# Kernel tuning notes

Hardware: AMD Instinct MI355X
Metric: run time of the kernel (lower is better)

Reference implementation:

```python
import jax, jax.numpy as jnp
import numpy as np

K = 3  # knnLoss default k


def _knn_loss(source_pc, target_pc, k=K):
    """Faithful translation of knnLoss.forward.

    For each batch: drop exact-zero (0,0,0) points from both clouds
    (emulated via masking for static shapes), find the k nearest *target*
    points for every *source* point (query=source, ref=target), take the
    mean Euclidean distance, then average over batch.
    """

    def per_batch(src, tgt):  # src, tgt: [N, 3]
        src_valid = jnp.any(src != 0.0, axis=-1)  # [Ns] move_zero_point mask
        tgt_valid = jnp.any(tgt != 0.0, axis=-1)  # [Nt]
        s2 = jnp.sum(src * src, axis=-1)          # [Ns]
        t2 = jnp.sum(tgt * tgt, axis=-1)          # [Nt]
        # squared pairwise distances, [Ns, Nt]
        d2 = s2[:, None] + t2[None, :] - 2.0 * (src @ tgt.T)
        d2 = jnp.maximum(d2, 0.0)
        # invalid (zero) target points can never be a neighbor
        d2 = jnp.where(tgt_valid[None, :], d2, jnp.inf)
        neg_top, _ = jax.lax.top_k(-d2, k)        # k smallest squared dists
        dist = jnp.sqrt(-neg_top)                 # [Ns, k] euclidean, like KNN_CUDA
        # mean over valid source points x k neighbors
        num = jnp.sum(jnp.where(src_valid[:, None], dist, 0.0))
        den = jnp.sum(src_valid).astype(dist.dtype) * k
        return num / den

    return jnp.mean(jax.vmap(per_batch)(source_pc, target_pc))


def setup_inputs() -> dict:
    key = jax.random.key(0)
    k1, k2 = jax.random.split(key)
    B, N = 4, 8192
    source_pc = jax.random.normal(k1, (B, N, 3), dtype=jnp.float32)
    target_pc = jax.random.normal(k2, (B, N, 3), dtype=jnp.float32)
    return {"source_pc": source_pc, "target_pc": target_pc}


def reference(source_pc, target_pc):
    return _knn_loss(source_pc, target_pc)
```

## Files before the change

### kernel.cpp

```cpp
#include <hip/hip_runtime.h>
#include <math.h>

#define BATCH 4
#define NPTS 8192
#define TILE 512
#define TSPLIT 16
#define SRC_PER_BLOCK 512
#define SRC_CHUNKS 16
#define NSRC_TOT (BATCH * NPTS)
#define NOCT (TILE / 8)
#define OCTF 36

typedef __attribute__((ext_vector_type(2))) float f2;

__device__ __forceinline__ float min3f(float a, float b, float c) {
    float d;
    asm("v_min3_f32 %0, %1, %2, %3" : "=v"(d) : "v"(a), "v"(b), "v"(c));
    return d;
}

__device__ __forceinline__ void insert3(float d, float& a0, float& a1, float& a2) {
    float h = fmaxf(a1, d);
    float m = __builtin_amdgcn_fmed3f(a0, a1, d);
    a2 = fminf(a2, h);
    a1 = m;
    a0 = fminf(a0, d);
}

__device__ __forceinline__ void merge33(float a0, float a1, float a2,
                                        float& b0, float& b1, float& b2) {
    float s0 = fminf(a0, b0);
    float h  = fmaxf(a0, b0);
    float m  = fminf(a1, b1);
    float mm = fminf(a2, b2);
    b1 = fminf(h, m);
    b2 = __builtin_amdgcn_fmed3f(h, m, mm);
    b0 = s0;
}

__device__ __forceinline__ void octet_insert(const float4* ob, f2 nx, f2 ny, f2 nz,
                                             float& c0, float& c1, float& c2) {
    float4 X0 = ob[0], X1 = ob[1], Y0 = ob[2], Y1 = ob[3];
    float4 Z0 = ob[4], Z1 = ob[5], W0 = ob[6], W1 = ob[7];
    f2 pa = __builtin_elementwise_fma((f2){Z0.x, Z0.y}, nz, (f2){W0.x, W0.y});
    pa = __builtin_elementwise_fma((f2){Y0.x, Y0.y}, ny, pa);
    pa = __builtin_elementwise_fma((f2){X0.x, X0.y}, nx, pa);
    f2 pb = __builtin_elementwise_fma((f2){Z0.z, Z0.w}, nz, (f2){W0.z, W0.w});
    pb = __builtin_elementwise_fma((f2){Y0.z, Y0.w}, ny, pb);
    pb = __builtin_elementwise_fma((f2){X0.z, X0.w}, nx, pb);
    f2 pc = __builtin_elementwise_fma((f2){Z1.x, Z1.y}, nz, (f2){W1.x, W1.y});
    pc = __builtin_elementwise_fma((f2){Y1.x, Y1.y}, ny, pc);
    pc = __builtin_elementwise_fma((f2){X1.x, X1.y}, nx, pc);
    f2 pd = __builtin_elementwise_fma((f2){Z1.z, Z1.w}, nz, (f2){W1.z, W1.w});
    pd = __builtin_elementwise_fma((f2){Y1.z, Y1.w}, ny, pd);
    pd = __builtin_elementwise_fma((f2){X1.z, X1.w}, nx, pd);
    insert3(pa.x, c0, c1, c2);
    insert3(pa.y, c0, c1, c2);
    insert3(pb.x, c0, c1, c2);
    insert3(pb.y, c0, c1, c2);
    insert3(pc.x, c0, c1, c2);
    insert3(pc.y, c0, c1, c2);
    insert3(pd.x, c0, c1, c2);
    insert3(pd.y, c0, c1, c2);
}

__global__ __launch_bounds__(256) void knn_partial(const float* __restrict__ src,
                                                   const float* __restrict__ tgt,
                                                   float* __restrict__ part,
                                                   float* __restrict__ hdr) {
    __shared__ float tsf[NOCT * OCTF];
    const int tid = threadIdx.x;
    const int sc = blockIdx.x, tc = blockIdx.y, b = blockIdx.z;

    if (sc == 0 && tc == 0 && b == 0 && tid < 16) hdr[tid] = 0.0f;

    {
        const float* tb = tgt + ((size_t)b * NPTS + (size_t)tc * TILE + 2 * tid) * 3;
        float x0 = tb[0], y0 = tb[1], z0 = tb[2];
        float x1 = tb[3], y1 = tb[4], z1 = tb[5];
        float w0 = x0 * x0 + y0 * y0 + z0 * z0;
        float w1 = x1 * x1 + y1 * y1 + z1 * z1;
        if (!(x0 != 0.f || y0 != 0.f || z0 != 0.f)) w0 = 3.0e38f;
        if (!(x1 != 0.f || y1 != 0.f || z1 != 0.f)) w1 = 3.0e38f;
        int o = tid >> 2;
        int k = (2 * tid) & 7;
        int base = o * OCTF + ((k >> 2) << 2) + (k & 3);
        *(float2*)(tsf + base)      = make_float2(x0, x1);
        *(float2*)(tsf + base + 8)  = make_float2(y0, y1);
        *(float2*)(tsf + base + 16) = make_float2(z0, z1);
        *(float2*)(tsf + base + 24) = make_float2(w0, w1);
    }
    __syncthreads();

    f2 nx[2], ny[2], nz[2];
    #pragma unroll
    for (int s = 0; s < 2; ++s) {
        int i = sc * SRC_PER_BLOCK + tid + 256 * s;
        const float* sp = src + ((size_t)b * NPTS + i) * 3;
        float ax = sp[0], ay = sp[1], az = sp[2];
        nx[s] = (f2){-2.f * ax, -2.f * ax};
        ny[s] = (f2){-2.f * ay, -2.f * ay};
        nz[s] = (f2){-2.f * az, -2.f * az};
    }

    float q0[2], q1[2], q2c[2];
    #pragma unroll
    for (int s = 0; s < 2; ++s) { q0[s] = q1[s] = q2c[s] = 3e38f; }

    const float4* tsv = (const float4*)tsf;
    #pragma unroll 2
    for (int o = 0; o < NOCT; ++o) {
        float4 X0 = tsv[9 * o + 0], X1 = tsv[9 * o + 1];
        float4 Y0 = tsv[9 * o + 2], Y1 = tsv[9 * o + 3];
        float4 Z0 = tsv[9 * o + 4], Z1 = tsv[9 * o + 5];
        float4 W0 = tsv[9 * o + 6], W1 = tsv[9 * o + 7];
        #pragma unroll
        for (int s = 0; s < 2; ++s) {
            f2 pa = __builtin_elementwise_fma((f2){Z0.x, Z0.y}, nz[s], (f2){W0.x, W0.y});
            pa = __builtin_elementwise_fma((f2){Y0.x, Y0.y}, ny[s], pa);
            pa = __builtin_elementwise_fma((f2){X0.x, X0.y}, nx[s], pa);
            f2 pb = __builtin_elementwise_fma((f2){Z0.z, Z0.w}, nz[s], (f2){W0.z, W0.w});
            pb = __builtin_elementwise_fma((f2){Y0.z, Y0.w}, ny[s], pb);
            pb = __builtin_elementwise_fma((f2){X0.z, X0.w}, nx[s], pb);
            f2 pc = __builtin_elementwise_fma((f2){Z1.x, Z1.y}, nz[s], (f2){W1.x, W1.y});
            pc = __builtin_elementwise_fma((f2){Y1.x, Y1.y}, ny[s], pc);
            pc = __builtin_elementwise_fma((f2){X1.x, X1.y}, nx[s], pc);
            f2 pd = __builtin_elementwise_fma((f2){Z1.z, Z1.w}, nz[s], (f2){W1.z, W1.w});
            pd = __builtin_elementwise_fma((f2){Y1.z, Y1.w}, ny[s], pd);
            pd = __builtin_elementwise_fma((f2){X1.z, X1.w}, nx[s], pd);
            float m1 = min3f(pa.x, pa.y, pb.x);
            float m2 = min3f(pb.y, pc.x, pc.y);
            float m3 = min3f(pd.x, pd.y, m1);
            float m4 = fminf(m2, m3);
            unsigned u = (__float_as_uint(m4) & 0xFFFFFFC0u) | (unsigned)o;
            insert3(__uint_as_float(u), q0[s], q1[s], q2c[s]);
        }
    }

    #pragma unroll
    for (int s = 0; s < 2; ++s) {
        float c0 = 3e38f, c1 = 3e38f, c2 = 3e38f;
        int o0 = (int)(__float_as_uint(q0[s]) & 63u);
        int o1 = (int)(__float_as_uint(q1[s]) & 63u);
        int o2 = (int)(__float_as_uint(q2c[s]) & 63u);
        octet_insert(tsv + 9 * o0, nx[s], ny[s], nz[s], c0, c1, c2);
        octet_insert(tsv + 9 * o1, nx[s], ny[s], nz[s], c0, c1, c2);
        octet_insert(tsv + 9 * o2, nx[s], ny[s], nz[s], c0, c1, c2);
        size_t flat = (size_t)b * NPTS + sc * SRC_PER_BLOCK + tid + 256 * s;
        part[((size_t)tc * 3 + 0) * NSRC_TOT + flat] = c0;
        part[((size_t)tc * 3 + 1) * NSRC_TOT + flat] = c1;
        part[((size_t)tc * 3 + 2) * NSRC_TOT + flat] = c2;
    }
}

__global__ __launch_bounds__(256) void knn_merge(const float* __restrict__ src,
                                                 const float* __restrict__ part,
                                                 float* __restrict__ acc,
                                                 float* __restrict__ cnt,
                                                 unsigned* __restrict__ ticket,
                                                 float* __restrict__ out) {
    const int gid = blockIdx.x * 256 + threadIdx.x;
    const int b = gid >> 13;

    float t0[4], t1[4], t2[4];
    #pragma unroll
    for (int c = 0; c < 4; ++c) { t0[c] = t1[c] = t2[c] = 3e38f; }
    #pragma unroll
    for (int q = 0; q < TSPLIT * 3; ++q)
        insert3(part[(size_t)q * NSRC_TOT + gid], t0[q & 3], t1[q & 3], t2[q & 3]);
    merge33(t0[1], t1[1], t2[1], t0[0], t1[0], t2[0]);
    merge33(t0[3], t1[3], t2[3], t0[2], t1[2], t2[2]);
    merge33(t0[2], t1[2], t2[2], t0[0], t1[0], t2[0]);

    float sx = src[(size_t)gid * 3 + 0];
    float sy = src[(size_t)gid * 3 + 1];
    float sz = src[(size_t)gid * 3 + 2];
    bool valid = (sx != 0.f) || (sy != 0.f) || (sz != 0.f);
    float qq = sx * sx + sy * sy + sz * sz;
    float s = valid ? (sqrtf(fmaxf(t0[0] + qq, 0.f)) + sqrtf(fmaxf(t1[0] + qq, 0.f)) +
                       sqrtf(fmaxf(t2[0] + qq, 0.f)))
                    : 0.f;
    float c = valid ? 1.f : 0.f;

    for (int off = 32; off >= 1; off >>= 1) {
        s += __shfl_down(s, off);
        c += __shfl_down(c, off);
    }
    __shared__ float red_s[4], red_c[4];
    int wave = threadIdx.x >> 6, lane = threadIdx.x & 63;
    if (lane == 0) { red_s[wave] = s; red_c[wave] = c; }
    __syncthreads();
    if (threadIdx.x == 0) {
        atomicAdd(&acc[b], red_s[0] + red_s[1] + red_s[2] + red_s[3]);
        atomicAdd(&cnt[b], red_c[0] + red_c[1] + red_c[2] + red_c[3]);
        __threadfence();
        unsigned t = atomicAdd(ticket, 1u);
        if (t == (unsigned)(gridDim.x - 1)) {
            float loss = 0.f;
            #pragma unroll
            for (int bb = 0; bb < BATCH; ++bb) {
                float as = atomicAdd(&acc[bb], 0.f);
                float ac = atomicAdd(&cnt[bb], 0.f);
                loss += as / (ac * 3.0f);
            }
            out[0] = loss * (1.0f / BATCH);
        }
    }
}

extern "C" void kernel_launch(void* const* d_in, const int* in_sizes, int n_in,
                              void* d_out, int out_size, void* d_ws, size_t ws_size,
                              hipStream_t stream) {
    const float* src = (const float*)d_in[0];
    const float* tgt = (const float*)d_in[1];
    float* out = (float*)d_out;

    float* hdr = (float*)d_ws;
    float* acc = hdr;
    float* cnt = hdr + 4;
    unsigned* ticket = (unsigned*)((char*)d_ws + 32);
    float* part = (float*)((char*)d_ws + 256);

    dim3 g1(SRC_CHUNKS, TSPLIT, BATCH);
    knn_partial<<<g1, 256, 0, stream>>>(src, tgt, part, hdr);

    knn_merge<<<dim3(NSRC_TOT / 256), 256, 0, stream>>>(src, part, acc, cnt, ticket, out);
}
```

Baseline: 98.78 us.

## Fuse partial KNN and merge into one kernel with per-wave target slots

Replaces the two-kernel scheme, which wrote per-tile top-3 partials to global memory and merged them in a second kernel, with a single kernel. Each block now handles 64 source points. Its four waves each scan a different quarter of the targets, staged through shared memory over four rounds, and the per-wave top-3 lists are merged in shared memory. This removes the partial-results buffer traffic and one launch, but each source point now gets one lane instead of two per thread, and the block does more serial rounds with extra syncs. A memset is added to zero the accumulators and ticket.

```diff
diff --git a/kernel.cpp b/kernel.cpp
--- a/kernel.cpp
+++ b/kernel.cpp
@@ -4,12 +4,14 @@
 #define BATCH 4
 #define NPTS 8192
 #define TILE 512
-#define TSPLIT 16
-#define SRC_PER_BLOCK 512
-#define SRC_CHUNKS 16
-#define NSRC_TOT (BATCH * NPTS)
-#define NOCT (TILE / 8)
+#define NTILES 16
+#define SLOTS 4
+#define ROUNDS 4
+#define SRC_PER_BLOCK 64
+#define NBLOCKS (BATCH * NPTS / SRC_PER_BLOCK)
+#define NOCT 64
 #define OCTF 36
+#define SLOTF (NOCT * OCTF)
 
 typedef __attribute__((ext_vector_type(2))) float f2;
 
@@ -64,146 +66,121 @@
     insert3(pd.y, c0, c1, c2);
 }
 
-__global__ __launch_bounds__(256) void knn_partial(const float* __restrict__ src,
-                                                   const float* __restrict__ tgt,
-                                                   float* __restrict__ part,
-                                                   float* __restrict__ hdr) {
-    __shared__ float tsf[NOCT * OCTF];
+__global__ __launch_bounds__(256) void knn_fused(const float* __restrict__ src,
+                                                 const float* __restrict__ tgt,
+                                                 float* __restrict__ acc,
+                                                 float* __restrict__ cnt,
+                                                 unsigned* __restrict__ ticket,
+                                                 float* __restrict__ out) {
+    __shared__ float tsf[SLOTS * SLOTF];
     const int tid = threadIdx.x;
-    const int sc = blockIdx.x, tc = blockIdx.y, b = blockIdx.z;
-
-    if (sc == 0 && tc == 0 && b == 0 && tid < 16) hdr[tid] = 0.0f;
-
-    {
-        const float* tb = tgt + ((size_t)b * NPTS + (size_t)tc * TILE + 2 * tid) * 3;
-        float x0 = tb[0], y0 = tb[1], z0 = tb[2];
-        float x1 = tb[3], y1 = tb[4], z1 = tb[5];
-        float w0 = x0 * x0 + y0 * y0 + z0 * z0;
-        float w1 = x1 * x1 + y1 * y1 + z1 * z1;
-        if (!(x0 != 0.f || y0 != 0.f || z0 != 0.f)) w0 = 3.0e38f;
-        if (!(x1 != 0.f || y1 != 0.f || z1 != 0.f)) w1 = 3.0e38f;
-        int o = tid >> 2;
-        int k = (2 * tid) & 7;
-        int base = o * OCTF + ((k >> 2) << 2) + (k & 3);
-        *(float2*)(tsf + base)      = make_float2(x0, x1);
-        *(float2*)(tsf + base + 8)  = make_float2(y0, y1);
-        *(float2*)(tsf + base + 16) = make_float2(z0, z1);
-        *(float2*)(tsf + base + 24) = make_float2(w0, w1);
-    }
-    __syncthreads();
-
-    f2 nx[2], ny[2], nz[2];
-    #pragma unroll
-    for (int s = 0; s < 2; ++s) {
-        int i = sc * SRC_PER_BLOCK + tid + 256 * s;
-        const float* sp = src + ((size_t)b * NPTS + i) * 3;
-        float ax = sp[0], ay = sp[1], az = sp[2];
-        nx[s] = (f2){-2.f * ax, -2.f * ax};
-        ny[s] = (f2){-2.f * ay, -2.f * ay};
-        nz[s] = (f2){-2.f * az, -2.f * az};
-    }
-
-    float q0[2], q1[2], q2c[2];
-    #pragma unroll
-    for (int s = 0; s < 2; ++s) { q0[s] = q1[s] = q2c[s] = 3e38f; }
-
-    const float4* tsv = (const float4*)tsf;
-    #pragma unroll 2
-    for (int o = 0; o < NOCT; ++o) {
-        float4 X0 = tsv[9 * o + 0], X1 = tsv[9 * o + 1];
-        float4 Y0 = tsv[9 * o + 2], Y1 = tsv[9 * o + 3];
-        float4 Z0 = tsv[9 * o + 4], Z1 = tsv[9 * o + 5];
-        float4 W0 = tsv[9 * o + 6], W1 = tsv[9 * o + 7];
+    const int lane = tid & 63, wave = tid >> 6;
+    const int bid = blockIdx.x;
+    const int gid = bid * SRC_PER_BLOCK + lane;
+    const int b = bid >> 7;
+
+    const float* sp = src + (size_t)gid * 3;
+    float ax = sp[0], ay = sp[1], az = sp[2];
+    f2 nx = (f2){-2.f * ax, -2.f * ax};
+    f2 ny = (f2){-2.f * ay, -2.f * ay};
+    f2 nz = (f2){-2.f * az, -2.f * az};
+
+    float e0 = 3e38f, e1 = 3e38f, e2 = 3e38f;
+
+    for (int r = 0; r < ROUNDS; ++r) {
+        __syncthreads();
         #pragma unroll
-        for (int s = 0; s < 2; ++s) {
-            f2 pa = __builtin_elementwise_fma((f2){Z0.x, Z0.y}, nz[s], (f2){W0.x, W0.y});
-            pa = __builtin_elementwise_fma((f2){Y0.x, Y0.y}, ny[s], pa);
-            pa = __builtin_elementwise_fma((f2){X0.x, X0.y}, nx[s], pa);
-            f2 pb = __builtin_elementwise_fma((f2){Z0.z, Z0.w}, nz[s], (f2){W0.z, W0.w});
-            pb = __builtin_elementwise_fma((f2){Y0.z, Y0.w}, ny[s], pb);
-            pb = __builtin_elementwise_fma((f2){X0.z, X0.w}, nx[s], pb);
-            f2 pc = __builtin_elementwise_fma((f2){Z1.x, Z1.y}, nz[s], (f2){W1.x, W1.y});
-            pc = __builtin_elementwise_fma((f2){Y1.x, Y1.y}, ny[s], pc);
-            pc = __builtin_elementwise_fma((f2){X1.x, X1.y}, nx[s], pc);
-            f2 pd = __builtin_elementwise_fma((f2){Z1.z, Z1.w}, nz[s], (f2){W1.z, W1.w});
-            pd = __builtin_elementwise_fma((f2){Y1.z, Y1.w}, ny[s], pd);
-            pd = __builtin_elementwise_fma((f2){X1.z, X1.w}, nx[s], pd);
+        for (int j = 0; j < 4; ++j) {
+            int p = j * 256 + tid;
+            const float* tb = tgt + ((size_t)b * NPTS + r * (SLOTS * TILE) + 2 * p) * 3;
+            float x0 = tb[0], y0 = tb[1], z0 = tb[2];
+            float x1 = tb[3], y1 = tb[4], z1 = tb[5];
+            float w0 = x0 * x0 + y0 * y0 + z0 * z0;
+            float w1 = x1 * x1 + y1 * y1 + z1 * z1;
+            if (!(x0 != 0.f || y0 != 0.f || z0 != 0.f)) w0 = 3.0e38f;
+            if (!(x1 != 0.f || y1 != 0.f || z1 != 0.f)) w1 = 3.0e38f;
+            int sl = p >> 8;
+            int o = (p >> 2) & 63;
+            int k = (2 * p) & 7;
+            int base = sl * SLOTF + o * OCTF + ((k >> 2) << 2) + (k & 3);
+            *(float2*)(tsf + base)      = make_float2(x0, x1);
+            *(float2*)(tsf + base + 8)  = make_float2(y0, y1);
+            *(float2*)(tsf + base + 16) = make_float2(z0, z1);
+            *(float2*)(tsf + base + 24) = make_float2(w0, w1);
+        }
+        __syncthreads();
+
+        const float4* tsv = (const float4*)(tsf + wave * SLOTF);
+        float q0 = 3e38f, q1 = 3e38f, q2 = 3e38f;
+        #pragma unroll 2
+        for (int o = 0; o < NOCT; ++o) {
+            float4 X0 = tsv[9 * o + 0], X1 = tsv[9 * o + 1];
+            float4 Y0 = tsv[9 * o + 2], Y1 = tsv[9 * o + 3];
+            float4 Z0 = tsv[9 * o + 4], Z1 = tsv[9 * o + 5];
+            float4 W0 = tsv[9 * o + 6], W1 = tsv[9 * o + 7];
+            f2 pa = __builtin_elementwise_fma((f2){Z0.x, Z0.y}, nz, (f2){W0.x, W0.y});
+            pa = __builtin_elementwise_fma((f2){Y0.x, Y0.y}, ny, pa);
+            pa = __builtin_elementwise_fma((f2){X0.x, X0.y}, nx, pa);
+            f2 pb = __builtin_elementwise_fma((f2){Z0.z, Z0.w}, nz, (f2){W0.z, W0.w});
+            pb = __builtin_elementwise_fma((f2){Y0.z, Y0.w}, ny, pb);
+            pb = __builtin_elementwise_fma((f2){X0.z, X0.w}, nx, pb);
+            f2 pc = __builtin_elementwise_fma((f2){Z1.x, Z1.y}, nz, (f2){W1.x, W1.y});
+            pc = __builtin_elementwise_fma((f2){Y1.x, Y1.y}, ny, pc);
+            pc = __builtin_elementwise_fma((f2){X1.x, X1.y}, nx, pc);
+            f2 pd = __builtin_elementwise_fma((f2){Z1.z, Z1.w}, nz, (f2){W1.z, W1.w});
+            pd = __builtin_elementwise_fma((f2){Y1.z, Y1.w}, ny, pd);
+            pd = __builtin_elementwise_fma((f2){X1.z, X1.w}, nx, pd);
             float m1 = min3f(pa.x, pa.y, pb.x);
             float m2 = min3f(pb.y, pc.x, pc.y);
             float m3 = min3f(pd.x, pd.y, m1);
             float m4 = fminf(m2, m3);
             unsigned u = (__float_as_uint(m4) & 0xFFFFFFC0u) | (unsigned)o;
-            insert3(__uint_as_float(u), q0[s], q1[s], q2c[s]);
-        }
+            insert3(__uint_as_float(u), q0, q1, q2);
+        }
+        octet_insert(tsv + 9 * (int)(__float_as_uint(q0) & 63u), nx, ny, nz, e0, e1, e2);
+        octet_insert(tsv + 9 * (int)(__float_as_uint(q1) & 63u), nx, ny, nz, e0, e1, e2);
+        octet_insert(tsv + 9 * (int)(__float_as_uint(q2) & 63u), nx, ny, nz, e0, e1, e2);
     }
 
-    #pragma unroll
-    for (int s = 0; s < 2; ++s) {
-        float c0 = 3e38f, c1 = 3e38f, c2 = 3e38f;
-        int o0 = (int)(__float_as_uint(q0[s]) & 63u);
-        int o1 = (int)(__float_as_uint(q1[s]) & 63u);
-        int o2 = (int)(__float_as_uint(q2c[s]) & 63u);
-        octet_insert(tsv + 9 * o0, nx[s], ny[s], nz[s], c0, c1, c2);
-        octet_insert(tsv + 9 * o1, nx[s], ny[s], nz[s], c0, c1, c2);
-        octet_insert(tsv + 9 * o2, nx[s], ny[s], nz[s], c0, c1, c2);
-        size_t flat = (size_t)b * NPTS + sc * SRC_PER_BLOCK + tid + 256 * s;
-        part[((size_t)tc * 3 + 0) * NSRC_TOT + flat] = c0;
-        part[((size_t)tc * 3 + 1) * NSRC_TOT + flat] = c1;
-        part[((size_t)tc * 3 + 2) * NSRC_TOT + flat] = c2;
-    }
-}
-
-__global__ __launch_bounds__(256) void knn_merge(const float* __restrict__ src,
-                                                 const float* __restrict__ part,
-                                                 float* __restrict__ acc,
-                                                 float* __restrict__ cnt,
-                                                 unsigned* __restrict__ ticket,
-                                                 float* __restrict__ out) {
-    const int gid = blockIdx.x * 256 + threadIdx.x;
-    const int b = gid >> 13;
-
-    float t0[4], t1[4], t2[4];
-    #pragma unroll
-    for (int c = 0; c < 4; ++c) { t0[c] = t1[c] = t2[c] = 3e38f; }
-    #pragma unroll
-    for (int q = 0; q < TSPLIT * 3; ++q)
-        insert3(part[(size_t)q * NSRC_TOT + gid], t0[q & 3], t1[q & 3], t2[q & 3]);
-    merge33(t0[1], t1[1], t2[1], t0[0], t1[0], t2[0]);
-    merge33(t0[3], t1[3], t2[3], t0[2], t1[2], t2[2]);
-    merge33(t0[2], t1[2], t2[2], t0[0], t1[0], t2[0]);
-
-    float sx = src[(size_t)gid * 3 + 0];
-    float sy = src[(size_t)gid * 3 + 1];
-    float sz = src[(size_t)gid * 3 + 2];
-    bool valid = (sx != 0.f) || (sy != 0.f) || (sz != 0.f);
-    float qq = sx * sx + sy * sy + sz * sz;
-    float s = valid ? (sqrtf(fmaxf(t0[0] + qq, 0.f)) + sqrtf(fmaxf(t1[0] + qq, 0.f)) +
-                       sqrtf(fmaxf(t2[0] + qq, 0.f)))
-                    : 0.f;
-    float c = valid ? 1.f : 0.f;
-
-    for (int off = 32; off >= 1; off >>= 1) {
-        s += __shfl_down(s, off);
-        c += __shfl_down(c, off);
-    }
-    __shared__ float red_s[4], red_c[4];
-    int wave = threadIdx.x >> 6, lane = threadIdx.x & 63;
-    if (lane == 0) { red_s[wave] = s; red_c[wave] = c; }
     __syncthreads();
-    if (threadIdx.x == 0) {
-        atomicAdd(&acc[b], red_s[0] + red_s[1] + red_s[2] + red_s[3]);
-        atomicAdd(&cnt[b], red_c[0] + red_c[1] + red_c[2] + red_c[3]);
-        __threadfence();
-        unsigned t = atomicAdd(ticket, 1u);
-        if (t == (unsigned)(gridDim.x - 1)) {
-            float loss = 0.f;
-            #pragma unroll
-            for (int bb = 0; bb < BATCH; ++bb) {
-                float as = atomicAdd(&acc[bb], 0.f);
-                float ac = atomicAdd(&cnt[bb], 0.f);
-                loss += as / (ac * 3.0f);
+    tsf[wave * 64 + lane]       = e0;
+    tsf[256 + wave * 64 + lane] = e1;
+    tsf[512 + wave * 64 + lane] = e2;
+    __syncthreads();
+
+    if (tid < 64) {
+        float a0 = tsf[lane], a1 = tsf[256 + lane], a2 = tsf[512 + lane];
+        #pragma unroll
+        for (int g = 1; g < 4; ++g)
+            merge33(tsf[g * 64 + lane], tsf[256 + g * 64 + lane],
+                    tsf[512 + g * 64 + lane], a0, a1, a2);
+
+        bool valid = (ax != 0.f) || (ay != 0.f) || (az != 0.f);
+        float qq = ax * ax + ay * ay + az * az;
+        float s = valid ? (sqrtf(fmaxf(a0 + qq, 0.f)) + sqrtf(fmaxf(a1 + qq, 0.f)) +
+                           sqrtf(fmaxf(a2 + qq, 0.f)))
+                        : 0.f;
+        float c = valid ? 1.f : 0.f;
+
+        for (int off = 32; off >= 1; off >>= 1) {
+            s += __shfl_down(s, off);
+            c += __shfl_down(c, off);
+        }
+        if (lane == 0) {
+            atomicAdd(&acc[b], s);
+            atomicAdd(&cnt[b], c);
+            __threadfence();
+            unsigned t = atomicAdd(ticket, 1u);
+            if (t == (unsigned)(NBLOCKS - 1)) {
+                float loss = 0.f;
+                #pragma unroll
+                for (int bb = 0; bb < BATCH; ++bb) {
+                    float as = atomicAdd(&acc[bb], 0.f);
+                    float ac = atomicAdd(&cnt[bb], 0.f);
+                    loss += as / (ac * 3.0f);
+                }
+                out[0] = loss * (1.0f / BATCH);
             }
-            out[0] = loss * (1.0f / BATCH);
         }
     }
 }
@@ -215,14 +192,10 @@
     const float* tgt = (const float*)d_in[1];
     float* out = (float*)d_out;
 
-    float* hdr = (float*)d_ws;
-    float* acc = hdr;
-    float* cnt = hdr + 4;
+    float* acc = (float*)d_ws;
+    float* cnt = acc + 4;
     unsigned* ticket = (unsigned*)((char*)d_ws + 32);
-    float* part = (float*)((char*)d_ws + 256);
-
-    dim3 g1(SRC_CHUNKS, TSPLIT, BATCH);
-    knn_partial<<<g1, 256, 0, stream>>>(src, tgt, part, hdr);
-
-    knn_merge<<<dim3(NSRC_TOT / 256), 256, 0, stream>>>(src, part, acc, cnt, ticket, out);
-}
+
+    hipMemsetAsync(d_ws, 0, 64, stream);
+    knn_fused<<<dim3(NBLOCKS), 256, 0, stream>>>(src, tgt, acc, cnt, ticket, out);
+}
```

After: 112.4 us. 1.14x slower.

## Fuse partial KNN and merge into one kernel with per-wave target tiles

Applied to the files above, without the earlier changes.

Replaces the two-kernel design (partial top-3 per target tile written to global memory, then a merge kernel) with a single 1024-thread block kernel. Each of 16 waves stages its own 512-point target tile in shared memory and computes top-3 for 128 source points, then the waves merge their results through shared memory before the reduction and atomics. This removes the global partial buffer traffic and the second launch, but adds a memsetAsync to reset the accumulators and uses 128 KB of shared memory per block, which limits occupancy. It also drops the padded octet stride (32 instead of 36 floats), which may introduce LDS bank conflicts.

```diff
diff --git a/kernel.cpp b/kernel.cpp
--- a/kernel.cpp
+++ b/kernel.cpp
@@ -4,12 +4,12 @@
 #define BATCH 4
 #define NPTS 8192
 #define TILE 512
-#define TSPLIT 16
-#define SRC_PER_BLOCK 512
-#define SRC_CHUNKS 16
-#define NSRC_TOT (BATCH * NPTS)
-#define NOCT (TILE / 8)
-#define OCTF 36
+#define NWAVES 16
+#define SRC_PER_BLOCK 128
+#define NBLOCKS (BATCH * NPTS / SRC_PER_BLOCK)
+#define NOCT 64
+#define OCTF 32
+#define SLOTF (NOCT * OCTF)
 
 typedef __attribute__((ext_vector_type(2))) float f2;
 
@@ -64,56 +64,61 @@
     insert3(pd.y, c0, c1, c2);
 }
 
-__global__ __launch_bounds__(256) void knn_partial(const float* __restrict__ src,
-                                                   const float* __restrict__ tgt,
-                                                   float* __restrict__ part,
-                                                   float* __restrict__ hdr) {
-    __shared__ float tsf[NOCT * OCTF];
+__global__ __launch_bounds__(1024, 4) void knn_fused(const float* __restrict__ src,
+                                                     const float* __restrict__ tgt,
+                                                     float* __restrict__ acc,
+                                                     float* __restrict__ cnt,
+                                                     unsigned* __restrict__ ticket,
+                                                     float* __restrict__ out) {
+    __shared__ float tsf[NWAVES * SLOTF];
     const int tid = threadIdx.x;
-    const int sc = blockIdx.x, tc = blockIdx.y, b = blockIdx.z;
-
-    if (sc == 0 && tc == 0 && b == 0 && tid < 16) hdr[tid] = 0.0f;
-
-    {
-        const float* tb = tgt + ((size_t)b * NPTS + (size_t)tc * TILE + 2 * tid) * 3;
-        float x0 = tb[0], y0 = tb[1], z0 = tb[2];
-        float x1 = tb[3], y1 = tb[4], z1 = tb[5];
-        float w0 = x0 * x0 + y0 * y0 + z0 * z0;
-        float w1 = x1 * x1 + y1 * y1 + z1 * z1;
-        if (!(x0 != 0.f || y0 != 0.f || z0 != 0.f)) w0 = 3.0e38f;
-        if (!(x1 != 0.f || y1 != 0.f || z1 != 0.f)) w1 = 3.0e38f;
-        int o = tid >> 2;
-        int k = (2 * tid) & 7;
-        int base = o * OCTF + ((k >> 2) << 2) + (k & 3);
-        *(float2*)(tsf + base)      = make_float2(x0, x1);
-        *(float2*)(tsf + base + 8)  = make_float2(y0, y1);
-        *(float2*)(tsf + base + 16) = make_float2(z0, z1);
-        *(float2*)(tsf + base + 24) = make_float2(w0, w1);
-    }
-    __syncthreads();
+    const int lane = tid & 63, wave = tid >> 6;
+    const int bid = blockIdx.x;
+    const int b = bid >> 6;
 
     f2 nx[2], ny[2], nz[2];
     #pragma unroll
     for (int s = 0; s < 2; ++s) {
-        int i = sc * SRC_PER_BLOCK + tid + 256 * s;
-        const float* sp = src + ((size_t)b * NPTS + i) * 3;
+        const float* sp = src + ((size_t)bid * SRC_PER_BLOCK + 64 * s + lane) * 3;
         float ax = sp[0], ay = sp[1], az = sp[2];
         nx[s] = (f2){-2.f * ax, -2.f * ax};
         ny[s] = (f2){-2.f * ay, -2.f * ay};
         nz[s] = (f2){-2.f * az, -2.f * az};
     }
 
+    {
+        const float* tb = tgt + ((size_t)b * NPTS + wave * TILE) * 3;
+        #pragma unroll
+        for (int j = 0; j < 4; ++j) {
+            int p = j * 64 + lane;
+            const float2* t2 = (const float2*)(tb + 6 * p);
+            float2 A = t2[0], Bv = t2[1], C = t2[2];
+            float x0 = A.x, y0 = A.y, z0 = Bv.x;
+            float x1 = Bv.y, y1 = C.x, z1 = C.y;
+            float w0 = x0 * x0 + y0 * y0 + z0 * z0;
+            float w1 = x1 * x1 + y1 * y1 + z1 * z1;
+            if (!(x0 != 0.f || y0 != 0.f || z0 != 0.f)) w0 = 3.0e38f;
+            if (!(x1 != 0.f || y1 != 0.f || z1 != 0.f)) w1 = 3.0e38f;
+            int o = p >> 2, k = (2 * p) & 7;
+            float* bp = tsf + wave * SLOTF + o * OCTF + k;
+            *(float2*)(bp)      = make_float2(x0, x1);
+            *(float2*)(bp + 8)  = make_float2(y0, y1);
+            *(float2*)(bp + 16) = make_float2(z0, z1);
+            *(float2*)(bp + 24) = make_float2(w0, w1);
+        }
+    }
+
     float q0[2], q1[2], q2c[2];
     #pragma unroll
     for (int s = 0; s < 2; ++s) { q0[s] = q1[s] = q2c[s] = 3e38f; }
 
-    const float4* tsv = (const float4*)tsf;
+    const float4* tsv = (const float4*)(tsf + wave * SLOTF);
     #pragma unroll 2
-    for (int o = 0; o < NOCT; ++o) {
-        float4 X0 = tsv[9 * o + 0], X1 = tsv[9 * o + 1];
-        float4 Y0 = tsv[9 * o + 2], Y1 = tsv[9 * o + 3];
-        float4 Z0 = tsv[9 * o + 4], Z1 = tsv[9 * o + 5];
-        float4 W0 = tsv[9 * o + 6], W1 = tsv[9 * o + 7];
+    for (int j = 0; j < NOCT; ++j) {
+        float4 X0 = tsv[8 * j + 0], X1 = tsv[8 * j + 1];
+        float4 Y0 = tsv[8 * j + 2], Y1 = tsv[8 * j + 3];
+        float4 Z0 = tsv[8 * j + 4], Z1 = tsv[8 * j + 5];
+        float4 W0 = tsv[8 * j + 6], W1 = tsv[8 * j + 7];
         #pragma unroll
         for (int s = 0; s < 2; ++s) {
             f2 pa = __builtin_elementwise_fma((f2){Z0.x, Z0.y}, nz[s], (f2){W0.x, W0.y});
@@ -132,70 +137,65 @@
             float m2 = min3f(pb.y, pc.x, pc.y);
             float m3 = min3f(pd.x, pd.y, m1);
             float m4 = fminf(m2, m3);
-            unsigned u = (__float_as_uint(m4) & 0xFFFFFFC0u) | (unsigned)o;
+            unsigned u = (__float_as_uint(m4) & 0xFFFFFFC0u) | (unsigned)j;
             insert3(__uint_as_float(u), q0[s], q1[s], q2c[s]);
         }
     }
 
+    float e0[2], e1[2], e2[2];
     #pragma unroll
     for (int s = 0; s < 2; ++s) {
-        float c0 = 3e38f, c1 = 3e38f, c2 = 3e38f;
-        int o0 = (int)(__float_as_uint(q0[s]) & 63u);
-        int o1 = (int)(__float_as_uint(q1[s]) & 63u);
-        int o2 = (int)(__float_as_uint(q2c[s]) & 63u);
-        octet_insert(tsv + 9 * o0, nx[s], ny[s], nz[s], c0, c1, c2);
-        octet_insert(tsv + 9 * o1, nx[s], ny[s], nz[s], c0, c1, c2);
-        octet_insert(tsv + 9 * o2, nx[s], ny[s], nz[s], c0, c1, c2);
-        size_t flat = (size_t)b * NPTS + sc * SRC_PER_BLOCK + tid + 256 * s;
-        part[((size_t)tc * 3 + 0) * NSRC_TOT + flat] = c0;
-        part[((size_t)tc * 3 + 1) * NSRC_TOT + flat] = c1;
-        part[((size_t)tc * 3 + 2) * NSRC_TOT + flat] = c2;
-    }
-}
-
-__global__ __launch_bounds__(256) void knn_merge(const float* __restrict__ src,
-                                                 const float* __restrict__ part,
-                                                 float* __restrict__ acc,
-                                                 float* __restrict__ cnt,
-                                                 unsigned* __restrict__ ticket,
-                                                 float* __restrict__ out) {
-    const int gid = blockIdx.x * 256 + threadIdx.x;
-    const int b = gid >> 13;
-
-    float t0[4], t1[4], t2[4];
-    #pragma unroll
-    for (int c = 0; c < 4; ++c) { t0[c] = t1[c] = t2[c] = 3e38f; }
-    #pragma unroll
-    for (int q = 0; q < TSPLIT * 3; ++q)
-        insert3(part[(size_t)q * NSRC_TOT + gid], t0[q & 3], t1[q & 3], t2[q & 3]);
-    merge33(t0[1], t1[1], t2[1], t0[0], t1[0], t2[0]);
-    merge33(t0[3], t1[3], t2[3], t0[2], t1[2], t2[2]);
-    merge33(t0[2], t1[2], t2[2], t0[0], t1[0], t2[0]);
-
-    float sx = src[(size_t)gid * 3 + 0];
-    float sy = src[(size_t)gid * 3 + 1];
-    float sz = src[(size_t)gid * 3 + 2];
-    bool valid = (sx != 0.f) || (sy != 0.f) || (sz != 0.f);
-    float qq = sx * sx + sy * sy + sz * sz;
-    float s = valid ? (sqrtf(fmaxf(t0[0] + qq, 0.f)) + sqrtf(fmaxf(t1[0] + qq, 0.f)) +
-                       sqrtf(fmaxf(t2[0] + qq, 0.f)))
-                    : 0.f;
-    float c = valid ? 1.f : 0.f;
-
-    for (int off = 32; off >= 1; off >>= 1) {
-        s += __shfl_down(s, off);
-        c += __shfl_down(c, off);
-    }
-    __shared__ float red_s[4], red_c[4];
-    int wave = threadIdx.x >> 6, lane = threadIdx.x & 63;
-    if (lane == 0) { red_s[wave] = s; red_c[wave] = c; }
+        e0[s] = 3e38f; e1[s] = 3e38f; e2[s] = 3e38f;
+        octet_insert(tsv + 8 * (int)(__float_as_uint(q0[s]) & 63u),
+                     nx[s], ny[s], nz[s], e0[s], e1[s], e2[s]);
+        octet_insert(tsv + 8 * (int)(__float_as_uint(q1[s]) & 63u),
+                     nx[s], ny[s], nz[s], e0[s], e1[s], e2[s]);
+        octet_insert(tsv + 8 * (int)(__float_as_uint(q2c[s]) & 63u),
+                     nx[s], ny[s], nz[s], e0[s], e1[s], e2[s]);
+    }
+
     __syncthreads();
-    if (threadIdx.x == 0) {
-        atomicAdd(&acc[b], red_s[0] + red_s[1] + red_s[2] + red_s[3]);
-        atomicAdd(&cnt[b], red_c[0] + red_c[1] + red_c[2] + red_c[3]);
-        __threadfence();
+    #pragma unroll
+    for (int s = 0; s < 2; ++s) {
+        int base = ((wave * 2 + s) * 64 + lane) * 3;
+        tsf[base]     = e0[s];
+        tsf[base + 1] = e1[s];
+        tsf[base + 2] = e2[s];
+    }
+    __syncthreads();
+
+    if (tid < 128) {
+        int l = tid & 63, srow = tid >> 6;
+        int base0 = ((0 * 2 + srow) * 64 + l) * 3;
+        float a0 = tsf[base0], a1 = tsf[base0 + 1], a2 = tsf[base0 + 2];
+        #pragma unroll
+        for (int w = 1; w < NWAVES; ++w) {
+            int bse = ((w * 2 + srow) * 64 + l) * 3;
+            merge33(tsf[bse], tsf[bse + 1], tsf[bse + 2], a0, a1, a2);
+        }
+        const float* sp = src + ((size_t)bid * SRC_PER_BLOCK + tid) * 3;
+        float sx = sp[0], sy = sp[1], sz = sp[2];
+        bool valid = (sx != 0.f) || (sy != 0.f) || (sz != 0.f);
+        float qq = sx * sx + sy * sy + sz * sz;
+        float sv = valid ? (sqrtf(fmaxf(a0 + qq, 0.f)) + sqrtf(fmaxf(a1 + qq, 0.f)) +
+                            sqrtf(fmaxf(a2 + qq, 0.f)))
+                         : 0.f;
+        float cv = valid ? 1.f : 0.f;
+        for (int off = 32; off >= 1; off >>= 1) {
+            sv += __shfl_down(sv, off);
+            cv += __shfl_down(cv, off);
+        }
+        if (l == 0) {
+            atomicAdd(&acc[b], sv);
+            atomicAdd(&cnt[b], cv);
+            __threadfence();
+        }
+    }
+    __syncthreads();
+
+    if (tid == 0) {
         unsigned t = atomicAdd(ticket, 1u);
-        if (t == (unsigned)(gridDim.x - 1)) {
+        if (t == (unsigned)(NBLOCKS - 1)) {
             float loss = 0.f;
             #pragma unroll
             for (int bb = 0; bb < BATCH; ++bb) {
@@ -215,14 +215,10 @@
     const float* tgt = (const float*)d_in[1];
     float* out = (float*)d_out;
 
-    float* hdr = (float*)d_ws;
-    float* acc = hdr;
-    float* cnt = hdr + 4;
+    float* acc = (float*)d_ws;
+    float* cnt = acc + 4;
     unsigned* ticket = (unsigned*)((char*)d_ws + 32);
-    float* part = (float*)((char*)d_ws + 256);
-
-    dim3 g1(SRC_CHUNKS, TSPLIT, BATCH);
-    knn_partial<<<g1, 256, 0, stream>>>(src, tgt, part, hdr);
-
-    knn_merge<<<dim3(NSRC_TOT / 256), 256, 0, stream>>>(src, part, acc, cnt, ticket, out);
-}
+
+    hipMemsetAsync(d_ws, 0, 64, stream);
+    knn_fused<<<dim3(NBLOCKS), 1024, 0, stream>>>(src, tgt, acc, cnt, ticket, out);
+}
```

Result: slower. 113.2 us (+14.6%).
